# Optimization experiments

Hardware: AMD Instinct MI355X
Metric: run time of the kernel (lower is better)

Reference implementation:

```python
import jax, jax.numpy as jnp
import numpy as np

N_CLUSTERS = 64
COLLAPSE_REG = 0.1
H_SMOOTH = -0.0001
H_ALPHA = 0.0001
H_LAMBDA = 0.0001


def setup_inputs() -> dict:
    key = jax.random.key(0)
    ks = jax.random.split(key, 6)
    n, d, k = 65536, 512, N_CLUSTERS
    e0 = 1048576  # directed edges before symmetrization
    features = jax.random.normal(ks[0], (n, d), jnp.float32)
    s = jax.random.randint(ks[1], (e0,), 0, n)
    t = jax.random.randint(ks[2], (e0,), 0, n)
    v = jax.random.uniform(ks[3], (e0,), jnp.float32)
    # symmetrize adjacency (real graph datasets are undirected -> L = D - A is PSD)
    edge_src = jnp.concatenate([s, t]).astype(jnp.int64)
    edge_dst = jnp.concatenate([t, s]).astype(jnp.int64)
    edge_vals = jnp.concatenate([v, v])
    W = jax.random.normal(ks[4], (d, k), jnp.float32) / np.sqrt(d).astype(np.float32)
    b = jnp.zeros((k,), jnp.float32)
    return dict(features=features, edge_src=edge_src, edge_dst=edge_dst,
                edge_vals=edge_vals, W=W, b=b)


def reference(features, edge_src, edge_dst, edge_vals, W, b):
    n, d = features.shape
    k = W.shape[1]
    # assignments = softmax(Dense(features))
    S = jax.nn.softmax(features @ W + b, axis=1)  # [n,k]
    cluster_sizes = jnp.sum(S, axis=0)            # [k]
    S_pool = S / cluster_sizes                    # [n,k]
    # sparse column-degree (tf.sparse.reduce_sum axis=0) and edge count
    deg_col = jax.ops.segment_sum(edge_vals, edge_dst, num_segments=n)[:, None]  # [n,1]
    m = jnp.sum(deg_col)
    # A @ S via edge-list gather/scatter (sparse_dense_matmul)
    AS = jax.ops.segment_sum(edge_vals[:, None] * S[edge_dst], edge_src,
                             num_segments=n)      # [n,k]
    graph_pooled = AS.T @ S                       # S^T A S, [k,k]
    normalizer = ((S.T @ deg_col) @ (deg_col.T @ S)) / 2.0 / m  # [k,k]
    spectral_loss = -jnp.trace(graph_pooled - normalizer) / 2.0 / m
    collapse_loss = (jnp.linalg.norm(cluster_sizes) / n
                     * jnp.sqrt(jnp.float32(k)) - 1.0)
    # pooled features
    FP = jax.nn.selu(S_pool.T @ features)         # [k,d]
    # FGC loss chain: Laplacian L = D_row - A applied sparsely
    deg_row = jax.ops.segment_sum(edge_vals, edge_src, num_segments=n)[:, None]
    LS = deg_row * S - AS                         # L @ S, [n,k]
    StLS = LS.T @ S                               # smoothness1 = S^T L S, [k,k]
    # log(det(StLS + ones)) computed stably via slogdet (det is positive: PSD + rank-1)
    _sign, logabsdet = jnp.linalg.slogdet(StLS + jnp.ones_like(StLS))
    smoothness_loss = logabsdet * H_SMOOTH
    # trace((L S) @ FP @ FP^T): trace of [n,k] matrix = sum of first k diagonal entries
    trace_loss = jnp.einsum('ic,cd,id->', LS[:k], FP, FP)
    frob_loss = jnp.linalg.norm(S @ FP - features) * H_ALPHA
    one_two_loss = jnp.linalg.norm(jnp.sum(jnp.abs(S), axis=0)) * H_LAMBDA
    fgc_loss = smoothness_loss + trace_loss + frob_loss + one_two_loss
    total_loss = spectral_loss + COLLAPSE_REG * collapse_loss + fgc_loss
    return FP, S, total_loss
```

## Files before the change

### kernel.cpp

```cpp
#include <hip/hip_runtime.h>
#include <hip/hip_bf16.h>
#include <cstdint>
#include <cstddef>

typedef unsigned short u16;
typedef float f32x4 __attribute__((ext_vector_type(4)));
typedef short bf16x8 __attribute__((ext_vector_type(8)));
typedef unsigned short u16x8 __attribute__((ext_vector_type(8)));

__device__ __forceinline__ u16 f2bf(float f) {
    uint32_t u = __float_as_uint(f);
    u += 0x7fffu + ((u >> 16) & 1u);
    return (u16)(u >> 16);
}
__device__ __forceinline__ float bf2f(u16 h) {
    return __uint_as_float(((uint32_t)h) << 16);
}

#define SWZ(c) ((((c) ^ ((c) >> 3)) & 7) << 2)
#define SWZ2(c) ((((c) >> 2) & 7) << 2)

__device__ __forceinline__ void softbar() {
    asm volatile("s_waitcnt lgkmcnt(0)" ::: "memory");
    __builtin_amdgcn_s_barrier();
    __builtin_amdgcn_sched_barrier(0);
}

__global__ __launch_bounds__(256) void k_prep(const float* __restrict__ Wg, u16* __restrict__ Wt) {
    int idx = blockIdx.x * 256 + threadIdx.x;
    int k = idx >> 6, c = idx & 63;
    int lin = c * 512 + (k ^ ((c & 7) << 3));
    Wt[lin] = f2bf(Wg[idx]);
}

__global__ __launch_bounds__(256) void k1(const float* __restrict__ F,
    const u16* __restrict__ WtG, const float* __restrict__ bias,
    float* __restrict__ S_out, u16* __restrict__ Sbf,
    float* __restrict__ sizes, float* __restrict__ scal) {
    __shared__ __align__(16) u16 Wl[64 * 512];
    __shared__ __align__(16) u16 Al[64 * 64];
    __shared__ float red4[4];
    const int tid = threadIdx.x;
    const int row0 = blockIdx.x * 64;
    for (int j = tid; j < 4096; j += 256)
        ((uint4*)Wl)[j] = ((const uint4*)WtG)[j];

    const int lane = tid & 63;
    const int wv = __builtin_amdgcn_readfirstlane(tid >> 6);
    const int l15 = lane & 15, lq = lane >> 4;
    f32x4 acc[4];
    #pragma unroll
    for (int tn = 0; tn < 4; tn++)
        #pragma unroll
        for (int e = 0; e < 4; e++) acc[tn][e] = 0.f;
    float sumf2 = 0.f;
    const int sr = tid >> 2, skq = tid & 3;
    const int sw = (sr & 7) << 3;

    for (int k0 = 0; k0 < 512; k0 += 64) {
        const float* fp = F + (size_t)(row0 + sr) * 512 + k0 + skq * 16;
        float4 v[4];
        u16 h[16];
        #pragma unroll
        for (int q = 0; q < 4; q++) v[q] = ((const float4*)fp)[q];
        #pragma unroll
        for (int q = 0; q < 4; q++) {
            sumf2 += v[q].x * v[q].x + v[q].y * v[q].y + v[q].z * v[q].z + v[q].w * v[q].w;
            h[q * 4 + 0] = f2bf(v[q].x); h[q * 4 + 1] = f2bf(v[q].y);
            h[q * 4 + 2] = f2bf(v[q].z); h[q * 4 + 3] = f2bf(v[q].w);
        }
        #pragma unroll
        for (int half = 0; half < 2; half++) {
            u16x8 pk;
            #pragma unroll
            for (int e2 = 0; e2 < 8; e2++) pk[e2] = h[half * 8 + e2];
            *(u16x8*)&Al[sr * 64 + ((skq * 16 + half * 8) ^ sw)] = pk;
        }
        __syncthreads();
        #pragma unroll
        for (int kk = 0; kk < 64; kk += 32) {
            const int arow = wv * 16 + l15;
            bf16x8 a = *(const bf16x8*)&Al[arow * 64 + ((kk + lq * 8) ^ ((arow & 7) << 3))];
            #pragma unroll
            for (int tn = 0; tn < 4; tn++) {
                const int bc = tn * 16 + l15;
                bf16x8 b = *(const bf16x8*)&Wl[bc * 512 + ((k0 + kk + lq * 8) ^ ((bc & 7) << 3))];
                acc[tn] = __builtin_amdgcn_mfma_f32_16x16x32_bf16(a, b, acc[tn], 0, 0, 0);
            }
        }
        __syncthreads();
    }

    float bias4[4], szacc[4] = {0.f, 0.f, 0.f, 0.f};
    #pragma unroll
    for (int tn = 0; tn < 4; tn++) bias4[tn] = bias[tn * 16 + l15];
    #pragma unroll
    for (int r2 = 0; r2 < 4; r2++) {
        float L[4];
        #pragma unroll
        for (int tn = 0; tn < 4; tn++) L[tn] = acc[tn][r2] + bias4[tn];
        float mx = fmaxf(fmaxf(L[0], L[1]), fmaxf(L[2], L[3]));
        #pragma unroll
        for (int mm = 1; mm < 16; mm <<= 1) mx = fmaxf(mx, __shfl_xor(mx, mm));
        float e[4], s = 0.f;
        #pragma unroll
        for (int tn = 0; tn < 4; tn++) { e[tn] = __expf(L[tn] - mx); s += e[tn]; }
        #pragma unroll
        for (int mm = 1; mm < 16; mm <<= 1) s += __shfl_xor(s, mm);
        const float inv = 1.f / s;
        const size_t grow = (size_t)(row0 + wv * 16 + lq * 4 + r2);
        #pragma unroll
        for (int tn = 0; tn < 4; tn++) {
            const float svl = e[tn] * inv;
            S_out[grow * 64 + tn * 16 + l15] = svl;
            Sbf[grow * 64 + tn * 16 + l15] = f2bf(svl);
            szacc[tn] += svl;
        }
    }
    #pragma unroll
    for (int tn = 0; tn < 4; tn++) {
        float vs = szacc[tn];
        vs += __shfl_xor(vs, 16);
        vs += __shfl_xor(vs, 32);
        if (lq == 0) atomicAdd(sizes + tn * 16 + l15, vs);
    }
    #pragma unroll
    for (int mm = 1; mm < 64; mm <<= 1) sumf2 += __shfl_xor(sumf2, mm);
    if (lane == 0) red4[wv] = sumf2;
    __syncthreads();
    if (tid == 0) atomicAdd(scal + 1, red4[0] + red4[1] + red4[2] + red4[3]);
}

__global__ __launch_bounds__(512) void k_mid(const int* __restrict__ esrc,
    const int* __restrict__ edst, const float* __restrict__ ev,
    const u16* __restrict__ Sbf, const float* __restrict__ S,
    const float* __restrict__ F, const int E2,
    float* __restrict__ GP8, float* __restrict__ SDS8, float* __restrict__ uv8,
    float* __restrict__ AS64, float* __restrict__ deg64, float* __restrict__ scal,
    float* __restrict__ G) {
    __shared__ uint32_t Tl[2][2048];
    __shared__ uint32_t Pl[2][2048];
    __shared__ uint32_t Ql[2][2048];
    __shared__ uint32_t Rl[2][2048];
    __shared__ uint32_t Ss2[2048];
    __shared__ uint32_t Fs2[4096];
    const int tid = threadIdx.x;
    const int lane = tid & 63;
    const int wv8 = __builtin_amdgcn_readfirstlane(tid >> 6);
    const int wv = wv8 & 7;
    const int l15 = lane & 15, lq = lane >> 4;
    const int xcd = blockIdx.x & 7;
    float* __restrict__ GPmy = GP8 + (size_t)xcd * 4096;
    float* __restrict__ SDSmy = SDS8 + (size_t)xcd * 4096;
    float* __restrict__ umy = uv8 + (size_t)xcd * 64;

    const bool isP = tid < 256;
    const int st = tid & 255;
    const int p = st >> 3, g = st & 7;
    float vsum = 0.f;
    float uacc[8];
    #pragma unroll
    for (int j = 0; j < 8; j++) uacc[j] = 0.f;
    f32x4 aG[2], aS[2];
    #pragma unroll
    for (int t = 0; t < 2; t++)
        #pragma unroll
        for (int r = 0; r < 4; r++) { aG[t][r] = 0.f; aS[t][r] = 0.f; }
    const int ma = 16 * (wv & 3) + l15;
    const int aoff = ma * 32, aswz = SWZ(ma);
    const int nb0 = 32 * ((wv & 7) >> 2) * 1 + 32 * (wv >> 2) * 0 + 32 * (wv >> 2) + l15;
    const int nb0r = 32 * (wv >> 2) + l15;
    const int nb1r = nb0r + 16;
    const int b0off = nb0r * 32, b0swz = SWZ(nb0r);
    const int b1off = nb1r * 32, b1swz = SWZ(nb1r);

    const int d0 = (blockIdx.x & 3) * 128;
    const int kblk = blockIdx.x >> 2;
    const int cwv = wv8 & 3, dh = wv8 >> 2;
    f32x4 acc2[4];
    #pragma unroll
    for (int t8 = 0; t8 < 4; t8++)
        #pragma unroll
        for (int r = 0; r < 4; r++) acc2[t8][r] = 0.f;
    const int s_ip = tid >> 3;
    const int s_cs = (tid & 7) * 8;
    const int tF = tid - 256;
    const int f_dg = tF & 31;
    const int f_ipb = tF >> 5;

    const int nch = E2 >> 6;
    const int stride = gridDim.x;
    int ch = blockIdx.x;
    const int sweep_left = (ch < nch) ? ((nch - ch + stride - 1) / stride) : 0;

    int2 ia_c, ib_c, ia_n, ib_n;
    float2 vv_c, vv_n;
    {
        const int e0 = (ch << 6) + 2 * p;
        ia_c = isP ? *(const int2*)&edst[e0] : *(const int2*)&esrc[e0];
        ib_c = isP ? *(const int2*)&esrc[e0] : *(const int2*)&edst[e0];
        vv_c = *(const float2*)&ev[e0];
    }
    u16x8 ra_c = *(const u16x8*)&Sbf[(size_t)ia_c.x * 64 + 8 * g];
    u16x8 rb_c = *(const u16x8*)&Sbf[(size_t)ia_c.y * 64 + 8 * g];
    int chn = ch + stride;
    {
        const int chc = chn < nch ? chn : (nch - 1);
        const int e0 = (chc << 6) + 2 * p;
        ia_n = isP ? *(const int2*)&edst[e0] : *(const int2*)&esrc[e0];
        ib_n = isP ? *(const int2*)&esrc[e0] : *(const int2*)&edst[e0];
        vv_n = *(const float2*)&ev[e0];
    }

    int buf = 0;
    int sw_done = 0, mm_done = 0;
    const int total = sweep_left + 8;
    for (int step = 0; step < total; step++) {
        const bool do_mm = (mm_done < 8) &&
                           ((sw_done >= (mm_done + 1) * 4) || (sw_done == sweep_left));
        if (do_mm) {
            const int i0 = kblk * 512 + mm_done * 64;
            if (isP) {
                const u16x8 r0 = *(const u16x8*)&Sbf[(size_t)(i0 + 2 * s_ip) * 64 + s_cs];
                const u16x8 r1 = *(const u16x8*)&Sbf[(size_t)(i0 + 2 * s_ip + 1) * 64 + s_cs];
                #pragma unroll
                for (int j = 0; j < 8; j++) {
                    const int c = s_cs + j;
                    Ss2[c * 32 + (s_ip ^ SWZ2(c))] =
                        (uint32_t)(u16)r0[j] | ((uint32_t)(u16)r1[j] << 16);
                }
            } else {
                #pragma unroll
                for (int s = 0; s < 4; s++) {
                    const int ip = f_ipb + 8 * s;
                    const float4 a = *(const float4*)(F + (size_t)(i0 + 2 * ip) * 512 + d0 + 4 * f_dg);
                    const float4 b = *(const float4*)(F + (size_t)(i0 + 2 * ip + 1) * 512 + d0 + 4 * f_dg);
                    const float al[4] = {a.x, a.y, a.z, a.w};
                    const float bl[4] = {b.x, b.y, b.z, b.w};
                    #pragma unroll
                    for (int j = 0; j < 4; j++) {
                        const int d = 4 * f_dg + j;
                        Fs2[d * 32 + (ip ^ SWZ2(d))] =
                            (uint32_t)f2bf(al[j]) | ((uint32_t)f2bf(bl[j]) << 16);
                    }
                }
            }
            softbar();
            #pragma unroll
            for (int kk = 0; kk < 64; kk += 32) {
                const int w0 = (kk >> 1) + (lq << 2);
                const int ca = 16 * cwv + l15;
                const bf16x8 afrag = *(const bf16x8*)&Ss2[ca * 32 + (w0 ^ SWZ2(ca))];
                #pragma unroll
                for (int t8r = 0; t8r < 4; t8r++) {
                    const int d = 16 * (4 * dh + t8r) + l15;
                    const bf16x8 bfrag = *(const bf16x8*)&Fs2[d * 32 + (w0 ^ SWZ2(d))];
                    acc2[t8r] = __builtin_amdgcn_mfma_f32_16x16x32_bf16(afrag, bfrag, acc2[t8r], 0, 0, 0);
                }
            }
            softbar();
            mm_done++;
        } else {
            if (isP) {
                #pragma unroll
                for (int j = 0; j < 8; j++) {
                    const int c = 8 * g + j;
                    const int off = c * 32 + (p ^ SWZ(c));
                    Tl[buf][off] = (uint32_t)(u16)ra_c[j] | ((uint32_t)(u16)rb_c[j] << 16);
                    Pl[buf][off] = (uint32_t)f2bf(vv_c.x * bf2f((u16)ra_c[j])) |
                                   ((uint32_t)f2bf(vv_c.y * bf2f((u16)rb_c[j])) << 16);
                }
            } else {
                #pragma unroll
                for (int j = 0; j < 8; j++) {
                    const int c = 8 * g + j;
                    const int off = c * 32 + (p ^ SWZ(c));
                    Ql[buf][off] = (uint32_t)(u16)ra_c[j] | ((uint32_t)(u16)rb_c[j] << 16);
                    Rl[buf][off] = (uint32_t)f2bf(vv_c.x * bf2f((u16)ra_c[j])) |
                                   ((uint32_t)f2bf(vv_c.y * bf2f((u16)rb_c[j])) << 16);
                }
            }
            #pragma unroll
            for (int j = 0; j < 8; j++)
                uacc[j] = fmaf(vv_c.x, bf2f((u16)ra_c[j]),
                          fmaf(vv_c.y, bf2f((u16)rb_c[j]), uacc[j]));
            if (!isP && g == 0) vsum += vv_c.x + vv_c.y;
            if (g == 0) {
                if (ib_c.x < 64) atomicAdd(deg64 + ib_c.x, vv_c.x);
                if (ib_c.y < 64) atomicAdd(deg64 + ib_c.y, vv_c.y);
            }
            if (ib_c.x < 64) {
                const float4 fa = *(const float4*)(S + (size_t)ia_c.x * 64 + 8 * g);
                const float4 fb = *(const float4*)(S + (size_t)ia_c.x * 64 + 8 * g + 4);
                float* dst = AS64 + ib_c.x * 64 + 8 * g;
                atomicAdd(dst + 0, vv_c.x * fa.x); atomicAdd(dst + 1, vv_c.x * fa.y);
                atomicAdd(dst + 2, vv_c.x * fa.z); atomicAdd(dst + 3, vv_c.x * fa.w);
                atomicAdd(dst + 4, vv_c.x * fb.x); atomicAdd(dst + 5, vv_c.x * fb.y);
                atomicAdd(dst + 6, vv_c.x * fb.z); atomicAdd(dst + 7, vv_c.x * fb.w);
            }
            if (ib_c.y < 64) {
                const float4 fa = *(const float4*)(S + (size_t)ia_c.y * 64 + 8 * g);
                const float4 fb = *(const float4*)(S + (size_t)ia_c.y * 64 + 8 * g + 4);
                float* dst = AS64 + ib_c.y * 64 + 8 * g;
                atomicAdd(dst + 0, vv_c.y * fa.x); atomicAdd(dst + 1, vv_c.y * fa.y);
                atomicAdd(dst + 2, vv_c.y * fa.z); atomicAdd(dst + 3, vv_c.y * fa.w);
                atomicAdd(dst + 4, vv_c.y * fb.x); atomicAdd(dst + 5, vv_c.y * fb.y);
                atomicAdd(dst + 6, vv_c.y * fb.z); atomicAdd(dst + 7, vv_c.y * fb.w);
            }
            const u16x8 ra_n = *(const u16x8*)&Sbf[(size_t)ia_n.x * 64 + 8 * g];
            const u16x8 rb_n = *(const u16x8*)&Sbf[(size_t)ia_n.y * 64 + 8 * g];
            const int chnn = chn + stride;
            int2 ia_nn, ib_nn;
            float2 vv_nn;
            {
                const int chc = chnn < nch ? chnn : (nch - 1);
                const int e0 = (chc << 6) + 2 * p;
                ia_nn = isP ? *(const int2*)&edst[e0] : *(const int2*)&esrc[e0];
                ib_nn = isP ? *(const int2*)&esrc[e0] : *(const int2*)&edst[e0];
                vv_nn = *(const float2*)&ev[e0];
            }
            softbar();
            #pragma unroll
            for (int half = 0; half < 2; half++) {
                const int w0 = half * 16 + lq * 4;
                const bf16x8 afP = *(const bf16x8*)&Pl[buf][aoff + (w0 ^ aswz)];
                const bf16x8 afR = *(const bf16x8*)&Rl[buf][aoff + (w0 ^ aswz)];
                const bf16x8 qb0 = *(const bf16x8*)&Ql[buf][b0off + (w0 ^ b0swz)];
                const bf16x8 qb1 = *(const bf16x8*)&Ql[buf][b1off + (w0 ^ b1swz)];
                const bf16x8 tb0 = *(const bf16x8*)&Tl[buf][b0off + (w0 ^ b0swz)];
                const bf16x8 tb1 = *(const bf16x8*)&Tl[buf][b1off + (w0 ^ b1swz)];
                aG[0] = __builtin_amdgcn_mfma_f32_16x16x32_bf16(afP, qb0, aG[0], 0, 0, 0);
                aG[1] = __builtin_amdgcn_mfma_f32_16x16x32_bf16(afP, qb1, aG[1], 0, 0, 0);
                aS[0] = __builtin_amdgcn_mfma_f32_16x16x32_bf16(afR, qb0, aS[0], 0, 0, 0);
                aS[1] = __builtin_amdgcn_mfma_f32_16x16x32_bf16(afR, qb1, aS[1], 0, 0, 0);
                aS[0] = __builtin_amdgcn_mfma_f32_16x16x32_bf16(afP, tb0, aS[0], 0, 0, 0);
                aS[1] = __builtin_amdgcn_mfma_f32_16x16x32_bf16(afP, tb1, aS[1], 0, 0, 0);
            }
            ch = chn;
            ia_c = ia_n; ib_c = ib_n; vv_c = vv_n; ra_c = ra_n; rb_c = rb_n;
            ia_n = ia_nn; ib_n = ib_nn; vv_n = vv_nn;
            chn = chnn;
            buf ^= 1;
            sw_done++;
        }
    }
    #pragma unroll
    for (int t = 0; t < 2; t++)
        #pragma unroll
        for (int r = 0; r < 4; r++) {
            const int c1 = 16 * (wv & 3) + 4 * lq + r;
            const int c2 = 32 * (wv >> 2) + 16 * t + l15;
            atomicAdd(GPmy + c1 * 64 + c2, aG[t][r]);
            atomicAdd(SDSmy + c1 * 64 + c2, aS[t][r]);
        }
    #pragma unroll
    for (int j = 0; j < 8; j++) {
        uacc[j] += __shfl_xor(uacc[j], 8);
        uacc[j] += __shfl_xor(uacc[j], 16);
        uacc[j] += __shfl_xor(uacc[j], 32);
    }
    if (lane < 8) {
        #pragma unroll
        for (int j = 0; j < 8; j++)
            atomicAdd(umy + 8 * lane + j, uacc[j]);
    }
    if (wv >= 4) {
        #pragma unroll
        for (int mm = 1; mm < 64; mm <<= 1) vsum += __shfl_xor(vsum, mm);
        if (lane == 0) atomicAdd(scal + 0, vsum + vsum);
    }
    #pragma unroll
    for (int t8r = 0; t8r < 4; t8r++)
        #pragma unroll
        for (int r = 0; r < 4; r++) {
            const int c = 16 * cwv + 4 * lq + r;
            const int d = d0 + 16 * (4 * dh + t8r) + l15;
            atomicAdd(G + (size_t)c * 512 + d, acc2[t8r][r]);
        }
}

__global__ __launch_bounds__(256) void k_mrg(const float* __restrict__ GP8,
    const float* __restrict__ SDS8, const float* __restrict__ uv8,
    float* __restrict__ GP, float* __restrict__ SDS, float* __restrict__ u_vec) {
    const int bid = blockIdx.x;
    const int t = threadIdx.x;
    if (bid < 16) {
        const int j = bid * 256 + t;
        const int jt = (j & 63) * 64 + (j >> 6);
        float s = 0.f;
        #pragma unroll
        for (int c = 0; c < 8; c++)
            s += GP8[(size_t)c * 4096 + j] + GP8[(size_t)c * 4096 + jt];
        GP[j] = s;
    } else if (bid < 32) {
        const int j = (bid - 16) * 256 + t;
        float s = 0.f;
        #pragma unroll
        for (int c = 0; c < 8; c++) s += SDS8[(size_t)c * 4096 + j];
        SDS[j] = s;
    } else if (t < 64) {
        float s = 0.f;
        #pragma unroll
        for (int c = 0; c < 8; c++) s += uv8[c * 64 + t];
        u_vec[t] = s;
    }
}

__global__ __launch_bounds__(256) void k_kk(const u16* __restrict__ Sbf,
    float* __restrict__ SS) {
    __shared__ float Pss[4][16][64];
    const int tid = threadIdx.x, lane = tid & 63;
    const int wv = __builtin_amdgcn_readfirstlane(tid >> 6);
    const int cs = blockIdx.x & 3, c0 = cs * 16;
    const int rbase = (blockIdx.x >> 2) * 512 + wv * 128;
    float ss[16];
    #pragma unroll
    for (int cc = 0; cc < 16; cc++) ss[cc] = 0.f;
    for (int r = 0; r < 128; r++) {
        const int i = rbase + r;
        const float sv = bf2f(Sbf[(size_t)i * 64 + lane]);
        const u16* srow = Sbf + (size_t)i * 64 + c0;
        #pragma unroll
        for (int cc = 0; cc < 16; cc++)
            ss[cc] = fmaf(bf2f(srow[cc]), sv, ss[cc]);
    }
    #pragma unroll
    for (int cc = 0; cc < 16; cc++) Pss[wv][cc][lane] = ss[cc];
    __syncthreads();
    for (int q = 0; q < 4; q++) {
        const int cell = tid * 4 + q, cc = cell >> 6, l = cell & 63;
        atomicAdd(SS + (c0 + cc) * 64 + l,
                  Pss[0][cc][l] + Pss[1][cc][l] + Pss[2][cc][l] + Pss[3][cc][l]);
    }
}

__device__ __forceinline__ float bred256(float v, float* red) {
    #pragma unroll
    for (int mm = 1; mm < 64; mm <<= 1) v += __shfl_xor(v, mm);
    const int t = threadIdx.x;
    __syncthreads();
    if ((t & 63) == 0) red[t >> 6] = v;
    __syncthreads();
    return red[0] + red[1] + red[2] + red[3];
}

__global__ __launch_bounds__(256) void k_fp(const float* __restrict__ G,
    const float* __restrict__ sizes, float* __restrict__ FP, float* __restrict__ scal) {
    __shared__ float red[4];
    const int idx = blockIdx.x * 256 + threadIdx.x;
    const int c = idx >> 9;
    const float g = G[idx];
    const float x = g / sizes[c];
    const float fp = 1.0507009873554805f * (x > 0.f ? x : 1.6732632423543772f * (__expf(x) - 1.f));
    FP[idx] = fp;
    const float gd = bred256(g * fp, red);
    if (threadIdx.x == 0) atomicAdd(scal + 2, gd);
}

__global__ __launch_bounds__(256) void k_fft(const float* __restrict__ FP, float* __restrict__ FFt) {
    __shared__ float red[256];
    const int c = blockIdx.x;
    const int cp = threadIdx.x & 63, part = threadIdx.x >> 6;
    float a = 0.f;
    const int dbase = part * 128;
    for (int dd = 0; dd < 128; dd++)
        a = fmaf(FP[c * 512 + dbase + dd], FP[cp * 512 + dbase + dd], a);
    red[threadIdx.x] = a;
    __syncthreads();
    if (threadIdx.x < 64)
        FFt[c * 64 + threadIdx.x] = red[threadIdx.x] + red[threadIdx.x + 64] +
                                    red[threadIdx.x + 128] + red[threadIdx.x + 192];
}

__global__ __launch_bounds__(256) void k_lu(const float* __restrict__ SDS,
    const float* __restrict__ GP, float* __restrict__ scal) {
    __shared__ float M[64][65];
    __shared__ float red[4];
    const int tid = threadIdx.x;
    const int l = tid & 63, q = tid >> 6;
    #pragma unroll
    for (int j = 0; j < 16; j++) {
        const int c = q * 16 + j;
        M[l][c] = SDS[l * 64 + c] - GP[l * 64 + c] + 1.0f;
    }
    __syncthreads();
    for (int k = 0; k < 63; k++) {
        if (l > k) {
            const float f = M[l][k] / M[k][k];
            const int cend = q * 16 + 16;
            for (int c = (q * 16 > k + 1 ? q * 16 : k + 1); c < cend; c++)
                M[l][c] = fmaf(-f, M[k][c], M[l][c]);
        }
        __syncthreads();
    }
    float v = (tid < 64) ? logf(fabsf(M[tid][tid])) : 0.f;
    const float ld = bred256(v, red);
    if (tid == 0) scal[3] = ld;
}

__global__ __launch_bounds__(256) void k_final(const float* __restrict__ GP,
    const float* __restrict__ SS, const float* __restrict__ FFt, const float* __restrict__ u_vec,
    const float* __restrict__ sizes, const float* __restrict__ deg64,
    const float* __restrict__ AS64, const float* __restrict__ S,
    const float* __restrict__ scal, float* __restrict__ out_loss, const float fn) {
    __shared__ float red[4];
    const int t = threadIdx.x;
    float sA = 0.f, trl = 0.f, trg = 0.f, u2 = 0.f, sz2 = 0.f;
    for (int q = t; q < 4096; q += 256) sA += SS[q] * FFt[q];
    for (int q = t; q < 4096; q += 256) {
        const int i = q >> 6, c = q & 63;
        const float ls = deg64[i] * S[i * 64 + c] - AS64[q];
        trl += ls * FFt[c * 64 + i];
    }
    if (t < 64) { trg = GP[t * 65]; u2 = u_vec[t] * u_vec[t]; sz2 = sizes[t] * sizes[t]; }
    sA = bred256(sA, red);
    trl = bred256(trl, red);
    trg = bred256(trg, red);
    u2 = bred256(u2, red);
    sz2 = bred256(sz2, red);
    if (t == 0) {
        const float m = scal[0], sumF2 = scal[1], gfp = scal[2], lad = scal[3];
        const float spectral = -(trg - u2 / (2.f * m)) / (2.f * m);
        const float collapse = sqrtf(sz2) / fn * 8.f - 1.f;
        const float frob = sqrtf(fmaxf(sA - 2.f * gfp + sumF2, 0.f)) * 1e-4f;
        const float one_two = sqrtf(sz2) * 1e-4f;
        const float smooth = lad * (-1e-4f);
        out_loss[0] = spectral + 0.1f * collapse + smooth + trl + frob + one_two;
    }
}

extern "C" void kernel_launch(void* const* d_in, const int* in_sizes, int n_in,
                              void* d_out, int out_size, void* d_ws, size_t ws_size,
                              hipStream_t stream) {
    const float* F = (const float*)d_in[0];
    const int* esrc = (const int*)d_in[1];
    const int* edst = (const int*)d_in[2];
    const float* ev = (const float*)d_in[3];
    const float* Wg = (const float*)d_in[4];
    const float* bg = (const float*)d_in[5];
    const int n = in_sizes[0] / 512;
    const int E = in_sizes[1];
    const int E2 = E >> 1;

    float* outF = (float*)d_out;
    float* outS = outF + 64 * 512;
    float* outL = outS + (size_t)n * 64;

    char* w = (char*)d_ws;
    float* sizes = (float*)w;
    float* u_vec = sizes + 64;
    float* scal = u_vec + 64;
    float* G = scal + 64;
    float* SS = G + 64 * 512;
    float* AS64 = SS + 4096;
    float* deg64 = AS64 + 4096;
    float* GP8 = deg64 + 64;
    float* SDS8 = GP8 + 8 * 4096;
    float* u8buf = SDS8 + 8 * 4096;
    char* zend = (char*)(u8buf + 512);
    const size_t zero_bytes = (size_t)(zend - w);
    float* GP = (float*)zend;
    float* SDS = GP + 4096;
    float* FFt = SDS + 4096;
    u16* Sbf = (u16*)(FFt + 4096);
    u16* Wt = Sbf + (size_t)n * 64;

    hipMemsetAsync(d_ws, 0, zero_bytes, stream);
    k_prep<<<128, 256, 0, stream>>>(Wg, Wt);
    k1<<<n / 64, 256, 0, stream>>>(F, Wt, bg, outS, Sbf, sizes, scal);
    k_mid<<<512, 512, 0, stream>>>(esrc, edst, ev, Sbf, outS, F, E2,
                                   GP8, SDS8, u8buf, AS64, deg64, scal, G);
    k_mrg<<<33, 256, 0, stream>>>(GP8, SDS8, u8buf, GP, SDS, u_vec);
    k_kk<<<(n / 512) * 4, 256, 0, stream>>>(Sbf, SS);
    k_fp<<<128, 256, 0, stream>>>(G, sizes, outF, scal);
    k_fft<<<64, 256, 0, stream>>>(outF, FFt);
    k_lu<<<1, 256, 0, stream>>>(SDS, GP, scal);
    k_final<<<1, 256, 0, stream>>>(GP, SS, FFt, u_vec, sizes, deg64, AS64, outS, scal, outL, (float)n);
}
```

Before: 466.4 us.

## Fold S^T S into k_mid MFMA pass and double k_mid grid

Removes the separate scalar k_kk kernel that computed S^T S and instead computes it with MFMA inside k_mid, reusing the S tile already staged in shared memory, on one block in eight. k_mid's grid doubles to 1024 blocks, with each block covering 64 feature columns instead of 128, and the interleaving of the feature matmul with the edge sweep is tightened accordingly. This cuts a kernel launch and a redundant read of S and shrinks LDS per block, which may allow more blocks per CU. In exchange, fewer edge chunks fall to each block and more atomics go to G, and blocks that also do S^T S carry extra work.

```diff
diff --git a/kernel.cpp b/kernel.cpp
--- a/kernel.cpp
+++ b/kernel.cpp
@@ -137,17 +137,17 @@
     const float* __restrict__ F, const int E2,
     float* __restrict__ GP8, float* __restrict__ SDS8, float* __restrict__ uv8,
     float* __restrict__ AS64, float* __restrict__ deg64, float* __restrict__ scal,
-    float* __restrict__ G) {
+    float* __restrict__ G, float* __restrict__ SS) {
     __shared__ uint32_t Tl[2][2048];
     __shared__ uint32_t Pl[2][2048];
     __shared__ uint32_t Ql[2][2048];
     __shared__ uint32_t Rl[2][2048];
     __shared__ uint32_t Ss2[2048];
-    __shared__ uint32_t Fs2[4096];
+    __shared__ uint32_t Fs2[2048];
     const int tid = threadIdx.x;
     const int lane = tid & 63;
     const int wv8 = __builtin_amdgcn_readfirstlane(tid >> 6);
-    const int wv = wv8 & 7;
+    const int wv = wv8;
     const int l15 = lane & 15, lq = lane >> 4;
     const int xcd = blockIdx.x & 7;
     float* __restrict__ GPmy = GP8 + (size_t)xcd * 4096;
@@ -161,32 +161,32 @@
     float uacc[8];
     #pragma unroll
     for (int j = 0; j < 8; j++) uacc[j] = 0.f;
-    f32x4 aG[2], aS[2];
+    f32x4 aG[2], aSd[2];
     #pragma unroll
     for (int t = 0; t < 2; t++)
         #pragma unroll
-        for (int r = 0; r < 4; r++) { aG[t][r] = 0.f; aS[t][r] = 0.f; }
+        for (int r = 0; r < 4; r++) { aG[t][r] = 0.f; aSd[t][r] = 0.f; }
     const int ma = 16 * (wv & 3) + l15;
     const int aoff = ma * 32, aswz = SWZ(ma);
-    const int nb0 = 32 * ((wv & 7) >> 2) * 1 + 32 * (wv >> 2) * 0 + 32 * (wv >> 2) + l15;
     const int nb0r = 32 * (wv >> 2) + l15;
     const int nb1r = nb0r + 16;
     const int b0off = nb0r * 32, b0swz = SWZ(nb0r);
     const int b1off = nb1r * 32, b1swz = SWZ(nb1r);
 
-    const int d0 = (blockIdx.x & 3) * 128;
-    const int kblk = blockIdx.x >> 2;
+    const int d0 = (blockIdx.x & 7) * 64;
+    const int kblk = blockIdx.x >> 3;
+    const bool doSS = (blockIdx.x & 7) == 0;
     const int cwv = wv8 & 3, dh = wv8 >> 2;
-    f32x4 acc2[4];
-    #pragma unroll
-    for (int t8 = 0; t8 < 4; t8++)
-        #pragma unroll
-        for (int r = 0; r < 4; r++) acc2[t8][r] = 0.f;
+    f32x4 acc2[2], aSS[2];
+    #pragma unroll
+    for (int t8 = 0; t8 < 2; t8++)
+        #pragma unroll
+        for (int r = 0; r < 4; r++) { acc2[t8][r] = 0.f; aSS[t8][r] = 0.f; }
     const int s_ip = tid >> 3;
     const int s_cs = (tid & 7) * 8;
     const int tF = tid - 256;
-    const int f_dg = tF & 31;
-    const int f_ipb = tF >> 5;
+    const int f_dg = tF & 15;
+    const int f_ipb = tF >> 4;
 
     const int nch = E2 >> 6;
     const int stride = gridDim.x;
@@ -217,7 +217,7 @@
     const int total = sweep_left + 8;
     for (int step = 0; step < total; step++) {
         const bool do_mm = (mm_done < 8) &&
-                           ((sw_done >= (mm_done + 1) * 4) || (sw_done == sweep_left));
+                           ((sw_done >= (mm_done + 1) * 2) || (sw_done == sweep_left));
         if (do_mm) {
             const int i0 = kblk * 512 + mm_done * 64;
             if (isP) {
@@ -231,8 +231,8 @@
                 }
             } else {
                 #pragma unroll
-                for (int s = 0; s < 4; s++) {
-                    const int ip = f_ipb + 8 * s;
+                for (int s = 0; s < 2; s++) {
+                    const int ip = f_ipb + 16 * s;
                     const float4 a = *(const float4*)(F + (size_t)(i0 + 2 * ip) * 512 + d0 + 4 * f_dg);
                     const float4 b = *(const float4*)(F + (size_t)(i0 + 2 * ip + 1) * 512 + d0 + 4 * f_dg);
                     const float al[4] = {a.x, a.y, a.z, a.w};
@@ -252,10 +252,18 @@
                 const int ca = 16 * cwv + l15;
                 const bf16x8 afrag = *(const bf16x8*)&Ss2[ca * 32 + (w0 ^ SWZ2(ca))];
                 #pragma unroll
-                for (int t8r = 0; t8r < 4; t8r++) {
-                    const int d = 16 * (4 * dh + t8r) + l15;
+                for (int t8r = 0; t8r < 2; t8r++) {
+                    const int d = 32 * dh + 16 * t8r + l15;
                     const bf16x8 bfrag = *(const bf16x8*)&Fs2[d * 32 + (w0 ^ SWZ2(d))];
                     acc2[t8r] = __builtin_amdgcn_mfma_f32_16x16x32_bf16(afrag, bfrag, acc2[t8r], 0, 0, 0);
+                }
+                if (doSS) {
+                    #pragma unroll
+                    for (int t8r = 0; t8r < 2; t8r++) {
+                        const int cb = 32 * dh + 16 * t8r + l15;
+                        const bf16x8 bS = *(const bf16x8*)&Ss2[cb * 32 + (w0 ^ SWZ2(cb))];
+                        aSS[t8r] = __builtin_amdgcn_mfma_f32_16x16x32_bf16(afrag, bS, aSS[t8r], 0, 0, 0);
+                    }
                 }
             }
             softbar();
@@ -331,10 +339,10 @@
                 const bf16x8 tb1 = *(const bf16x8*)&Tl[buf][b1off + (w0 ^ b1swz)];
                 aG[0] = __builtin_amdgcn_mfma_f32_16x16x32_bf16(afP, qb0, aG[0], 0, 0, 0);
                 aG[1] = __builtin_amdgcn_mfma_f32_16x16x32_bf16(afP, qb1, aG[1], 0, 0, 0);
-                aS[0] = __builtin_amdgcn_mfma_f32_16x16x32_bf16(afR, qb0, aS[0], 0, 0, 0);
-                aS[1] = __builtin_amdgcn_mfma_f32_16x16x32_bf16(afR, qb1, aS[1], 0, 0, 0);
-                aS[0] = __builtin_amdgcn_mfma_f32_16x16x32_bf16(afP, tb0, aS[0], 0, 0, 0);
-                aS[1] = __builtin_amdgcn_mfma_f32_16x16x32_bf16(afP, tb1, aS[1], 0, 0, 0);
+                aSd[0] = __builtin_amdgcn_mfma_f32_16x16x32_bf16(afR, qb0, aSd[0], 0, 0, 0);
+                aSd[1] = __builtin_amdgcn_mfma_f32_16x16x32_bf16(afR, qb1, aSd[1], 0, 0, 0);
+                aSd[0] = __builtin_amdgcn_mfma_f32_16x16x32_bf16(afP, tb0, aSd[0], 0, 0, 0);
+                aSd[1] = __builtin_amdgcn_mfma_f32_16x16x32_bf16(afP, tb1, aSd[1], 0, 0, 0);
             }
             ch = chn;
             ia_c = ia_n; ib_c = ib_n; vv_c = vv_n; ra_c = ra_n; rb_c = rb_n;
@@ -351,7 +359,7 @@
             const int c1 = 16 * (wv & 3) + 4 * lq + r;
             const int c2 = 32 * (wv >> 2) + 16 * t + l15;
             atomicAdd(GPmy + c1 * 64 + c2, aG[t][r]);
-            atomicAdd(SDSmy + c1 * 64 + c2, aS[t][r]);
+            atomicAdd(SDSmy + c1 * 64 + c2, aSd[t][r]);
         }
     #pragma unroll
     for (int j = 0; j < 8; j++) {
@@ -370,13 +378,23 @@
         if (lane == 0) atomicAdd(scal + 0, vsum + vsum);
     }
     #pragma unroll
-    for (int t8r = 0; t8r < 4; t8r++)
+    for (int t8r = 0; t8r < 2; t8r++)
         #pragma unroll
         for (int r = 0; r < 4; r++) {
             const int c = 16 * cwv + 4 * lq + r;
-            const int d = d0 + 16 * (4 * dh + t8r) + l15;
+            const int d = d0 + 32 * dh + 16 * t8r + l15;
             atomicAdd(G + (size_t)c * 512 + d, acc2[t8r][r]);
         }
+    if (doSS) {
+        #pragma unroll
+        for (int t8r = 0; t8r < 2; t8r++)
+            #pragma unroll
+            for (int r = 0; r < 4; r++) {
+                const int c = 16 * cwv + 4 * lq + r;
+                const int d = 32 * dh + 16 * t8r + l15;
+                atomicAdd(SS + c * 64 + d, aSS[t8r][r]);
+            }
+    }
 }
 
 __global__ __launch_bounds__(256) void k_mrg(const float* __restrict__ GP8,
@@ -403,34 +421,6 @@
         #pragma unroll
         for (int c = 0; c < 8; c++) s += uv8[c * 64 + t];
         u_vec[t] = s;
-    }
-}
-
-__global__ __launch_bounds__(256) void k_kk(const u16* __restrict__ Sbf,
-    float* __restrict__ SS) {
-    __shared__ float Pss[4][16][64];
-    const int tid = threadIdx.x, lane = tid & 63;
-    const int wv = __builtin_amdgcn_readfirstlane(tid >> 6);
-    const int cs = blockIdx.x & 3, c0 = cs * 16;
-    const int rbase = (blockIdx.x >> 2) * 512 + wv * 128;
-    float ss[16];
-    #pragma unroll
-    for (int cc = 0; cc < 16; cc++) ss[cc] = 0.f;
-    for (int r = 0; r < 128; r++) {
-        const int i = rbase + r;
-        const float sv = bf2f(Sbf[(size_t)i * 64 + lane]);
-        const u16* srow = Sbf + (size_t)i * 64 + c0;
-        #pragma unroll
-        for (int cc = 0; cc < 16; cc++)
-            ss[cc] = fmaf(bf2f(srow[cc]), sv, ss[cc]);
-    }
-    #pragma unroll
-    for (int cc = 0; cc < 16; cc++) Pss[wv][cc][lane] = ss[cc];
-    __syncthreads();
-    for (int q = 0; q < 4; q++) {
-        const int cell = tid * 4 + q, cc = cell >> 6, l = cell & 63;
-        atomicAdd(SS + (c0 + cc) * 64 + l,
-                  Pss[0][cc][l] + Pss[1][cc][l] + Pss[2][cc][l] + Pss[3][cc][l]);
     }
 }
 
@@ -568,10 +558,9 @@
     hipMemsetAsync(d_ws, 0, zero_bytes, stream);
     k_prep<<<128, 256, 0, stream>>>(Wg, Wt);
     k1<<<n / 64, 256, 0, stream>>>(F, Wt, bg, outS, Sbf, sizes, scal);
-    k_mid<<<512, 512, 0, stream>>>(esrc, edst, ev, Sbf, outS, F, E2,
-                                   GP8, SDS8, u8buf, AS64, deg64, scal, G);
+    k_mid<<<1024, 512, 0, stream>>>(esrc, edst, ev, Sbf, outS, F, E2,
+                                    GP8, SDS8, u8buf, AS64, deg64, scal, G, SS);
     k_mrg<<<33, 256, 0, stream>>>(GP8, SDS8, u8buf, GP, SDS, u_vec);
-    k_kk<<<(n / 512) * 4, 256, 0, stream>>>(Sbf, SS);
     k_fp<<<128, 256, 0, stream>>>(G, sizes, outF, scal);
     k_fft<<<64, 256, 0, stream>>>(outF, FFt);
     k_lu<<<1, 256, 0, stream>>>(SDS, GP, scal);
```

New measurement: 551.5 us. +18.3%, slower.
